# Optimization experiments

Hardware: AMD Instinct MI355X
Metric: run time of the kernel (lower is better)

Reference implementation:

```python
import jax, jax.numpy as jnp
import numpy as np

D_MODEL = 1024
N_BLOCKS = 4
D_STATE = 16
D_CONV = 4
EXPAND = 2
DT_RANK = 64  # ceil(1024/16)
D_INNER = EXPAND * D_MODEL
BATCH = 2
SEQLEN = 1024


def setup_inputs() -> dict:
    key = jax.random.key(0)
    ks = jax.random.split(key, 8)
    s = 0.02
    f = lambda k, sh: (jax.random.normal(k, sh, dtype=jnp.float32) * s)
    return {
        "x": jax.random.normal(ks[0], (BATCH, SEQLEN, D_MODEL), dtype=jnp.float32),
        "norm_w": jnp.ones((N_BLOCKS, D_MODEL), jnp.float32),
        "norm_b": jnp.zeros((N_BLOCKS, D_MODEL), jnp.float32),
        "in_proj_w": f(ks[1], (N_BLOCKS, D_MODEL, 2 * D_INNER)),
        "conv_w": f(ks[2], (N_BLOCKS, D_INNER, D_CONV)),
        "conv_b": jnp.zeros((N_BLOCKS, D_INNER), jnp.float32),
        "xproj_w": f(ks[3], (N_BLOCKS, D_INNER, DT_RANK + 2 * D_STATE)),
        "dtproj_w": f(ks[4], (N_BLOCKS, DT_RANK, D_INNER)),
        "dtproj_b": jnp.full((N_BLOCKS, D_INNER), -4.6, jnp.float32),  # softplus ~ 0.01
        "A_log": jnp.tile(jnp.log(jnp.arange(1, D_STATE + 1, dtype=jnp.float32))[None, None, :], (N_BLOCKS, D_INNER, 1)),
        "skip_D": jnp.ones((N_BLOCKS, D_INNER), jnp.float32),
        "out_proj_w": f(ks[5], (N_BLOCKS, D_INNER, D_MODEL)),
        "fn_w": jnp.ones((D_MODEL,), jnp.float32),
        "fn_b": jnp.zeros((D_MODEL,), jnp.float32),
    }


def _layer_norm(x, w, b):
    m = jnp.mean(x, -1, keepdims=True)
    v = jnp.mean((x - m) ** 2, -1, keepdims=True)
    return (x - m) * jax.lax.rsqrt(v + 1e-5) * w + b


def _selective_scan(u, dt, A, Bm, Cm, Dp):
    # u, dt: (B,L,E)  A: (E,N)  Bm, Cm: (B,L,N)  Dp: (E,)
    dA = jnp.exp(dt[..., None] * A)                 # (B,L,E,N) ZOH discretization of A
    dBu = (dt * u)[..., None] * Bm[:, :, None, :]   # (B,L,E,N) Euler discretization of B*u

    def step(h, inp):
        dA_t, dBu_t, C_t = inp
        h = dA_t * h + dBu_t                        # (B,E,N)
        y = jnp.einsum('ben,bn->be', h, C_t)
        return h, y

    h0 = jnp.zeros((u.shape[0], u.shape[2], A.shape[1]), u.dtype)
    xs = (jnp.moveaxis(dA, 1, 0), jnp.moveaxis(dBu, 1, 0), jnp.moveaxis(Cm, 1, 0))
    _, ys = jax.lax.scan(step, h0, xs)
    y = jnp.moveaxis(ys, 0, 1)                      # (B,L,E)
    return y + u * Dp


def _mamba(x, in_w, cw, cb, xw, dtw, dtb, A_log, Dp, ow):
    L = x.shape[1]
    xz = x @ in_w                                   # (B,L,2E)
    u, z = jnp.split(xz, 2, axis=-1)
    K = cw.shape[1]
    up = jnp.pad(u, ((0, 0), (K - 1, 0), (0, 0)))   # causal depthwise conv
    conv = cb + sum(up[:, k:k + L, :] * cw[:, k] for k in range(K))
    u = jax.nn.silu(conv)
    dbl = u @ xw                                    # (B,L,R+2N)
    dt = jax.nn.softplus(dbl[..., :DT_RANK] @ dtw + dtb)
    Bm = dbl[..., DT_RANK:DT_RANK + D_STATE]
    Cm = dbl[..., DT_RANK + D_STATE:]
    A = -jnp.exp(A_log)
    y = _selective_scan(u, dt, A, Bm, Cm, Dp)
    y = y * jax.nn.silu(z)                          # gating branch
    return y @ ow


def _forward(x, norm_w, norm_b, in_proj_w, conv_w, conv_b, xproj_w, dtproj_w, dtproj_b, A_log, skip_D, out_proj_w, fn_w, fn_b):
    for i in range(N_BLOCKS):
        h = _layer_norm(x, norm_w[i], norm_b[i])
        h = _mamba(h, in_proj_w[i], conv_w[i], conv_b[i], xproj_w[i], dtproj_w[i], dtproj_b[i], A_log[i], skip_D[i], out_proj_w[i])
        x = x + h                                   # pre-norm residual
    return _layer_norm(x, fn_w, fn_b)


def reference(x, norm_w, norm_b, in_proj_w, conv_w, conv_b, xproj_w, dtproj_w, dtproj_b, A_log, skip_D, out_proj_w, fn_w, fn_b):
    return _forward(x, norm_w, norm_b, in_proj_w, conv_w, conv_b, xproj_w, dtproj_w, dtproj_b, A_log, skip_D, out_proj_w, fn_w, fn_b)
```

## Files before the change

kernel.cpp:

```cpp
#include <hip/hip_runtime.h>
#include <hip/hip_bf16.h>
#include <math.h>

#define BATCH 2
#define SEQLEN 1024
#define DMODEL 1024
#define DINNER 2048
#define DSTATE 16
#define DTRANK 64
#define XDIM 96
#define KCONV 4
#define NBLOCKS 4
#define MROWS (BATCH*SEQLEN)

#define NCHUNK 64
#define CLEN (SEQLEN/NCHUNK)
#define SUN 4

typedef short bf16x8 __attribute__((ext_vector_type(8)));
typedef unsigned short u16x8 __attribute__((ext_vector_type(8)));
typedef float f32x4 __attribute__((ext_vector_type(4)));

__device__ __forceinline__ unsigned short f2bf(float x) {
    union { float f; unsigned u; } c; c.f = x;
    unsigned r = c.u + 0x7FFFu + ((c.u >> 16) & 1u);
    return (unsigned short)(r >> 16);
}
__device__ __forceinline__ float bf2f(unsigned short h) {
    union { unsigned u; float f; } c; c.u = (unsigned)h << 16;
    return c.f;
}

__device__ __forceinline__ void gload16(const void* src, void* dst) {
    __builtin_amdgcn_global_load_lds(
        (const __attribute__((address_space(1))) void*)src,
        (__attribute__((address_space(3))) void*)dst, 16, 0, 0);
}

__global__ __launch_bounds__(256) void lnc_k(const float* __restrict__ x,
    const float* __restrict__ w, const float* __restrict__ b,
    float* __restrict__ resid, unsigned short* __restrict__ out)
{
    int row = blockIdx.x;
    int tid = threadIdx.x;
    size_t off = (size_t)row * DMODEL + tid * 4;
    float4 v = *(const float4*)(x + off);
    *(float4*)(resid + off) = v;
    float s  = v.x + v.y + v.z + v.w;
    float sq = v.x*v.x + v.y*v.y + v.z*v.z + v.w*v.w;
    #pragma unroll
    for (int o = 32; o > 0; o >>= 1) {
        s  += __shfl_down(s, o);
        sq += __shfl_down(sq, o);
    }
    __shared__ float ss[4], sq4[4];
    int wid = tid >> 6;
    if ((tid & 63) == 0) { ss[wid] = s; sq4[wid] = sq; }
    __syncthreads();
    if (tid == 0) {
        ss[0]  = ss[0] + ss[1] + ss[2] + ss[3];
        sq4[0] = sq4[0] + sq4[1] + sq4[2] + sq4[3];
    }
    __syncthreads();
    float mean = ss[0] * (1.0f / DMODEL);
    float var  = sq4[0] * (1.0f / DMODEL) - mean * mean;
    float rstd = rsqrtf(var + 1e-5f);
    float4 wv = *(const float4*)(w + tid * 4);
    float4 bv = *(const float4*)(b + tid * 4);
    ushort4 h;
    h.x = f2bf((v.x - mean) * rstd * wv.x + bv.x);
    h.y = f2bf((v.y - mean) * rstd * wv.y + bv.y);
    h.z = f2bf((v.z - mean) * rstd * wv.z + bv.z);
    h.w = f2bf((v.w - mean) * rstd * wv.w + bv.w);
    *(ushort4*)(out + off) = h;
}

template<int FINAL>
__global__ __launch_bounds__(256) void predln_k(
    const float* __restrict__ pout, float* __restrict__ resid,
    const float* __restrict__ w, const float* __restrict__ b,
    unsigned short* __restrict__ hb16, float* __restrict__ fout)
{
    int row = blockIdx.x;
    int tid = threadIdx.x;
    const size_t MN = (size_t)MROWS * DMODEL;
    size_t off = (size_t)row * DMODEL + tid * 4;
    float4 p0 = *(const float4*)(pout + off);
    float4 p1 = *(const float4*)(pout + off + MN);
    float4 p2 = *(const float4*)(pout + off + 2 * MN);
    float4 p3 = *(const float4*)(pout + off + 3 * MN);
    float4 r  = *(const float4*)(resid + off);
    float4 v;
    v.x = r.x + (p0.x + p1.x) + (p2.x + p3.x);
    v.y = r.y + (p0.y + p1.y) + (p2.y + p3.y);
    v.z = r.z + (p0.z + p1.z) + (p2.z + p3.z);
    v.w = r.w + (p0.w + p1.w) + (p2.w + p3.w);
    if (!FINAL) *(float4*)(resid + off) = v;

    float s  = v.x + v.y + v.z + v.w;
    float sq = v.x*v.x + v.y*v.y + v.z*v.z + v.w*v.w;
    #pragma unroll
    for (int o = 32; o > 0; o >>= 1) {
        s  += __shfl_down(s, o);
        sq += __shfl_down(sq, o);
    }
    __shared__ float ss[4], sq4[4];
    int wid = tid >> 6;
    if ((tid & 63) == 0) { ss[wid] = s; sq4[wid] = sq; }
    __syncthreads();
    if (tid == 0) {
        ss[0]  = ss[0] + ss[1] + ss[2] + ss[3];
        sq4[0] = sq4[0] + sq4[1] + sq4[2] + sq4[3];
    }
    __syncthreads();
    float mean = ss[0] * (1.0f / DMODEL);
    float var  = sq4[0] * (1.0f / DMODEL) - mean * mean;
    float rstd = rsqrtf(var + 1e-5f);
    float4 wv = *(const float4*)(w + tid * 4);
    float4 bv = *(const float4*)(b + tid * 4);
    float o0 = (v.x - mean) * rstd * wv.x + bv.x;
    float o1 = (v.y - mean) * rstd * wv.y + bv.y;
    float o2 = (v.z - mean) * rstd * wv.z + bv.z;
    float o3 = (v.w - mean) * rstd * wv.w + bv.w;
    if (FINAL) {
        *(float4*)(fout + off) = make_float4(o0, o1, o2, o3);
    } else {
        ushort4 h;
        h.x = f2bf(o0); h.y = f2bf(o1); h.z = f2bf(o2); h.w = f2bf(o3);
        *(ushort4*)(hb16 + off) = h;
    }
}

__global__ __launch_bounds__(256) void wtr2_k(
    const float* __restrict__ W, unsigned short* __restrict__ WT,
    int N, int K, long long wstride, long long wtstride)
{
    const float* Wl = W + (size_t)blockIdx.z * wstride;
    unsigned short* WTl = WT + (size_t)blockIdx.z * wtstride;
    __shared__ float T[64][65];
    int n0 = blockIdx.x * 64, k0 = blockIdx.y * 64;
    int tid = threadIdx.x;
    int kk = tid >> 4, nn = (tid & 15) * 4;
    #pragma unroll
    for (int p = 0; p < 4; ++p) {
        float4 v = make_float4(0.f, 0.f, 0.f, 0.f);
        if (n0 + nn + 4 <= N)
            v = *(const float4*)(Wl + (size_t)(k0 + p * 16 + kk) * N + n0 + nn);
        T[p * 16 + kk][nn + 0] = v.x;
        T[p * 16 + kk][nn + 1] = v.y;
        T[p * 16 + kk][nn + 2] = v.z;
        T[p * 16 + kk][nn + 3] = v.w;
    }
    __syncthreads();
    int n2 = tid >> 4, k2 = (tid & 15) * 4;
    #pragma unroll
    for (int p = 0; p < 4; ++p) {
        int nrow = n0 + p * 16 + n2;
        ushort4 h = {0, 0, 0, 0};
        if (nrow < N) {
            h.x = f2bf(T[k2 + 0][p * 16 + n2]);
            h.y = f2bf(T[k2 + 1][p * 16 + n2]);
            h.z = f2bf(T[k2 + 2][p * 16 + n2]);
            h.w = f2bf(T[k2 + 3][p * 16 + n2]);
        }
        *(ushort4*)(WTl + (size_t)nrow * K + k0 + k2) = h;
    }
}

template<int EPI, int BN>
__global__ __launch_bounds__(256) void mgemm6_k(
    const unsigned short* __restrict__ A,
    const unsigned short* __restrict__ BT,
    float* __restrict__ out0, float* __restrict__ out1,
    const float* __restrict__ bias,
    int N, int Kf, int Kloc)
{
    constexpr int WN = BN / 2;
    constexpr int NJ = WN / 16;
    __shared__ unsigned short As[3][128 * 32];
    __shared__ unsigned short Bs[3][BN * 32];
    int tid = threadIdx.x;
    int lane = tid & 63, w = tid >> 6;
    int wr = w >> 1, wc = w & 1;
    int m0 = blockIdx.y * 128, n0 = blockIdx.x * BN;
    int lr = lane & 15, G = lane >> 4;

    int ra0 = w * 32 + (lane >> 2);
    int ra1 = ra0 + 16;
    int ga0 = (lane & 3) ^ ((ra0 >> 1) & 3);
    int ga1 = (lane & 3) ^ ((ra1 >> 1) & 3);
    int rb0 = w * (BN / 4) + (lane >> 2);
    int gb0 = (lane & 3) ^ ((rb0 >> 1) & 3);
    int rb1 = rb0 + 16;
    int gb1 = (lane & 3) ^ ((rb1 >> 1) & 3);

    int kz = blockIdx.z * Kloc;
    const unsigned short* pa0 = A  + (size_t)(m0 + ra0) * Kf + kz + ga0 * 8;
    const unsigned short* pa1 = A  + (size_t)(m0 + ra1) * Kf + kz + ga1 * 8;
    const unsigned short* pb0 = BT + (size_t)(n0 + rb0) * Kf + kz + gb0 * 8;
    const unsigned short* pb1 = BT + (size_t)(n0 + rb1) * Kf + kz + gb1 * 8;
    int dA0 = (w * 32) * 32, dA1 = dA0 + 16 * 32;
    int dB0 = (w * (BN / 4)) * 32, dB1 = dB0 + 16 * 32;

#define ISSUE(tt, bufi) do {                                   \
        gload16(pa0 + (tt) * 32, &As[bufi][dA0]);              \
        gload16(pa1 + (tt) * 32, &As[bufi][dA1]);              \
        gload16(pb0 + (tt) * 32, &Bs[bufi][dB0]);              \
        if (BN == 128) gload16(pb1 + (tt) * 32, &Bs[bufi][dB1]); \
    } while (0)

    f32x4 acc[4][NJ] = {};
    int T = Kloc / 32;

    ISSUE(0, 0);
    if (T > 1) ISSUE(1, 1);

    int cur = 0;
    for (int t = 0; t < T; ++t) {
        if (t + 1 < T) {
            if constexpr (BN == 128)
                asm volatile("s_waitcnt vmcnt(4)" ::: "memory");
            else
                asm volatile("s_waitcnt vmcnt(3)" ::: "memory");
        } else {
            asm volatile("s_waitcnt vmcnt(0)" ::: "memory");
        }
        __builtin_amdgcn_s_barrier();
        if (t + 2 < T) {
            int nb = cur + 2; if (nb >= 3) nb -= 3;
            ISSUE(t + 2, nb);
        }
        bf16x8 af[4], bfr[NJ];
        #pragma unroll
        for (int i = 0; i < 4; ++i) {
            int r = wr * 64 + i * 16 + lr;
            af[i] = *(const bf16x8*)&As[cur][r * 32 + ((G ^ ((r >> 1) & 3)) << 3)];
        }
        #pragma unroll
        for (int j = 0; j < NJ; ++j) {
            int r = wc * WN + j * 16 + lr;
            bfr[j] = *(const bf16x8*)&Bs[cur][r * 32 + ((G ^ ((r >> 1) & 3)) << 3)];
        }
        #pragma unroll
        for (int i = 0; i < 4; ++i)
            #pragma unroll
            for (int j = 0; j < NJ; ++j)
                acc[i][j] = __builtin_amdgcn_mfma_f32_16x16x32_bf16(
                    af[i], bfr[j], acc[i][j], 0, 0, 0);
        __builtin_amdgcn_s_barrier();
        cur = (cur + 1 == 3) ? 0 : cur + 1;
    }
#undef ISSUE

    int rbase = m0 + wr * 64 + (lane >> 4) * 4;
    int cbase = n0 + wc * WN + lr;
    #pragma unroll
    for (int i = 0; i < 4; ++i)
        #pragma unroll
        for (int j = 0; j < NJ; ++j)
            #pragma unroll
            for (int r = 0; r < 4; ++r) {
                int row = rbase + i * 16 + r;
                int col = cbase + j * 16;
                float c = acc[i][j][r];
                if (EPI == 0) {
                    if (col < DINNER)
                        ((unsigned short*)out0)[(size_t)row * DINNER + col] = f2bf(c);
                    else
                        ((unsigned short*)out1)[(size_t)row * DINNER + (col - DINNER)] = f2bf(c);
                } else if (EPI == 2) {
                    out0[(size_t)blockIdx.z * MROWS * N + (size_t)row * N + col] = c;
                } else if (EPI == 3) {
                    if (col < XDIM)
                        out0[(size_t)blockIdx.z * MROWS * XDIM +
                             (size_t)row * XDIM + col] = c;
                } else {
                    float cc = c + bias[col];
                    cc = fmaxf(cc, 0.f) + log1pf(__expf(-fabsf(cc)));
                    ((unsigned short*)out0)[(size_t)row * N + col] = f2bf(cc);
                }
            }
}

#define XSPLIT 16
__global__ __launch_bounds__(256) void xprojR_k(
    const float* __restrict__ part, float* __restrict__ dbl,
    unsigned short* __restrict__ db64)
{
    int idx = blockIdx.x * 256 + threadIdx.x;
    float s = 0.f;
    #pragma unroll
    for (int k = 0; k < XSPLIT; ++k)
        s += part[(size_t)k * MROWS * XDIM + idx];
    dbl[idx] = s;
    int col = idx % XDIM;
    if (col < DTRANK)
        db64[(size_t)(idx / XDIM) * DTRANK + col] = f2bf(s);
}

__global__ __launch_bounds__(256) void conv_k(const unsigned short* __restrict__ u,
    const float* __restrict__ cw, const float* __restrict__ cb,
    unsigned short* __restrict__ out)
{
    int idx = blockIdx.x * 256 + threadIdx.x;
    int c8 = idx & (DINNER / 8 - 1);
    int t  = (idx >> 8) & (SEQLEN - 1);
    int b  = idx >> 18;
    int e0 = c8 * 8;
    size_t base = (size_t)b * SEQLEN * DINNER + (size_t)t * DINNER + e0;
    u16x8 rows[KCONV];
    #pragma unroll
    for (int k = 0; k < KCONV; ++k) {
        int tt = t + k - (KCONV - 1);
        u16x8 zv = {0,0,0,0,0,0,0,0};
        rows[k] = (tt >= 0) ?
            *(const u16x8*)(u + base + (size_t)(k - (KCONV - 1)) * DINNER) : zv;
    }
    u16x8 o;
    #pragma unroll
    for (int j = 0; j < 8; ++j) {
        float4 wv = *(const float4*)(cw + (size_t)(e0 + j) * KCONV);
        float acc = cb[e0 + j];
        acc = fmaf(bf2f(rows[0][j]), wv.x, acc);
        acc = fmaf(bf2f(rows[1][j]), wv.y, acc);
        acc = fmaf(bf2f(rows[2][j]), wv.z, acc);
        acc = fmaf(bf2f(rows[3][j]), wv.w, acc);
        o[j] = f2bf(acc / (1.f + __expf(-acc)));
    }
    *(u16x8*)(out + base) = o;
}

template<int CTRL>
__device__ __forceinline__ float qadd(float x) {
    int y = __builtin_amdgcn_update_dpp(0, __float_as_int(x), CTRL, 0xF, 0xF, true);
    return x + __int_as_float(y);
}

__global__ __launch_bounds__(1024, 8) void scan_k(
    const unsigned short* __restrict__ dt, const unsigned short* __restrict__ uc,
    const float* __restrict__ dbl, const unsigned short* __restrict__ z,
    const float* __restrict__ A_log, const float* __restrict__ Dp,
    unsigned short* __restrict__ yout)
{
    __shared__ float sAlo[NCHUNK][8][2][4], sAhi[NCHUNK][8][2][4];
    __shared__ float sBlo[NCHUNK][8][2][4], sBhi[NCHUNK][8][2][4];
    int tid = threadIdx.x;
    int sub = tid & 1;
    int ei  = (tid >> 1) & 7;
    int ch  = tid >> 4;
    int bid = blockIdx.x;
    int blk = (bid & 7) * 64 + (bid >> 3);
    int eg  = blk & 255;
    int b   = blk >> 8;
    int e   = eg * 8 + ei;

    const float L2E = 1.4426950408889634f;
    float AstL2[8];
    {
        const float* ap = A_log + (size_t)e * DSTATE + sub * 8;
        #pragma unroll
        for (int q = 0; q < 2; ++q) {
            float4 v = *(const float4*)(ap + q * 4);
            AstL2[q * 4 + 0] = -__expf(v.x) * L2E;
            AstL2[q * 4 + 1] = -__expf(v.y) * L2E;
            AstL2[q * 4 + 2] = -__expf(v.z) * L2E;
            AstL2[q * 4 + 3] = -__expf(v.w) * L2E;
        }
    }
    size_t base_e = (size_t)b * SEQLEN * DINNER + e;
    size_t base_x = (size_t)b * SEQLEN * XDIM + DTRANK + sub * 8;
    int t0c = ch * CLEN;

    float h[8] = {0.f, 0.f, 0.f, 0.f, 0.f, 0.f, 0.f, 0.f};
    float ssum = 0.f;
    for (int t0 = t0c; t0 < t0c + CLEN; t0 += SUN) {
        float sdt[SUN], su[SUN];
        #pragma unroll
        for (int u = 0; u < SUN; ++u) {
            size_t te = base_e + (size_t)(t0 + u) * DINNER;
            sdt[u] = bf2f(dt[te]);
            su[u]  = bf2f(uc[te]);
        }
        #pragma unroll
        for (int u = 0; u < SUN; ++u) {
            const float* dx = dbl + base_x + (size_t)(t0 + u) * XDIM;
            float4 bn0 = *(const float4*)(dx);
            float4 bn1 = *(const float4*)(dx + 4);
            float dtu = sdt[u] * su[u];
            ssum += sdt[u];
            h[0] = fmaf(__builtin_amdgcn_exp2f(sdt[u] * AstL2[0]), h[0], dtu * bn0.x);
            h[1] = fmaf(__builtin_amdgcn_exp2f(sdt[u] * AstL2[1]), h[1], dtu * bn0.y);
            h[2] = fmaf(__builtin_amdgcn_exp2f(sdt[u] * AstL2[2]), h[2], dtu * bn0.z);
            h[3] = fmaf(__builtin_amdgcn_exp2f(sdt[u] * AstL2[3]), h[3], dtu * bn0.w);
            h[4] = fmaf(__builtin_amdgcn_exp2f(sdt[u] * AstL2[4]), h[4], dtu * bn1.x);
            h[5] = fmaf(__builtin_amdgcn_exp2f(sdt[u] * AstL2[5]), h[5], dtu * bn1.y);
            h[6] = fmaf(__builtin_amdgcn_exp2f(sdt[u] * AstL2[6]), h[6], dtu * bn1.z);
            h[7] = fmaf(__builtin_amdgcn_exp2f(sdt[u] * AstL2[7]), h[7], dtu * bn1.w);
        }
    }
    float a_[8];
    #pragma unroll
    for (int i = 0; i < 8; ++i) a_[i] = __builtin_amdgcn_exp2f(AstL2[i] * ssum);
    *(f32x4*)&sAlo[ch][ei][sub][0] = *(f32x4*)&a_[0];
    *(f32x4*)&sAhi[ch][ei][sub][0] = *(f32x4*)&a_[4];
    *(f32x4*)&sBlo[ch][ei][sub][0] = *(f32x4*)&h[0];
    *(f32x4*)&sBhi[ch][ei][sub][0] = *(f32x4*)&h[4];
    __syncthreads();

    #pragma unroll
    for (int s = 1; s < NCHUNK; s <<= 1) {
        float pa[8], pb[8];
        bool act = (ch >= s);
        if (act) {
            *(f32x4*)&pa[0] = *(const f32x4*)&sAlo[ch - s][ei][sub][0];
            *(f32x4*)&pa[4] = *(const f32x4*)&sAhi[ch - s][ei][sub][0];
            *(f32x4*)&pb[0] = *(const f32x4*)&sBlo[ch - s][ei][sub][0];
            *(f32x4*)&pb[4] = *(const f32x4*)&sBhi[ch - s][ei][sub][0];
        }
        __syncthreads();
        if (act) {
            #pragma unroll
            for (int i = 0; i < 8; ++i) {
                h[i]  = fmaf(a_[i], pb[i], h[i]);
                a_[i] *= pa[i];
            }
            *(f32x4*)&sAlo[ch][ei][sub][0] = *(f32x4*)&a_[0];
            *(f32x4*)&sAhi[ch][ei][sub][0] = *(f32x4*)&a_[4];
            *(f32x4*)&sBlo[ch][ei][sub][0] = *(f32x4*)&h[0];
            *(f32x4*)&sBhi[ch][ei][sub][0] = *(f32x4*)&h[4];
        }
        __syncthreads();
    }

    if (ch > 0) {
        *(f32x4*)&h[0] = *(const f32x4*)&sBlo[ch - 1][ei][sub][0];
        *(f32x4*)&h[4] = *(const f32x4*)&sBhi[ch - 1][ei][sub][0];
    } else {
        #pragma unroll
        for (int i = 0; i < 8; ++i) h[i] = 0.f;
    }

    float Dk = Dp[e];
    for (int t0 = t0c; t0 < t0c + CLEN; t0 += SUN) {
        float sdt[SUN], su[SUN], zz[SUN];
        #pragma unroll
        for (int u = 0; u < SUN; ++u) {
            size_t te = base_e + (size_t)(t0 + u) * DINNER;
            sdt[u] = bf2f(dt[te]);
            su[u]  = bf2f(uc[te]);
            zz[u]  = bf2f(z[te]);
        }
        #pragma unroll
        for (int u = 0; u < SUN; ++u) {
            const float* dx = dbl + base_x + (size_t)(t0 + u) * XDIM;
            float4 bn0 = *(const float4*)(dx);
            float4 bn1 = *(const float4*)(dx + 4);
            float4 cn0 = *(const float4*)(dx + 16);
            float4 cn1 = *(const float4*)(dx + 20);
            float dtu = sdt[u] * su[u];
            h[0] = fmaf(__builtin_amdgcn_exp2f(sdt[u] * AstL2[0]), h[0], dtu * bn0.x);
            h[1] = fmaf(__builtin_amdgcn_exp2f(sdt[u] * AstL2[1]), h[1], dtu * bn0.y);
            h[2] = fmaf(__builtin_amdgcn_exp2f(sdt[u] * AstL2[2]), h[2], dtu * bn0.z);
            h[3] = fmaf(__builtin_amdgcn_exp2f(sdt[u] * AstL2[3]), h[3], dtu * bn0.w);
            h[4] = fmaf(__builtin_amdgcn_exp2f(sdt[u] * AstL2[4]), h[4], dtu * bn1.x);
            h[5] = fmaf(__builtin_amdgcn_exp2f(sdt[u] * AstL2[5]), h[5], dtu * bn1.y);
            h[6] = fmaf(__builtin_amdgcn_exp2f(sdt[u] * AstL2[6]), h[6], dtu * bn1.z);
            h[7] = fmaf(__builtin_amdgcn_exp2f(sdt[u] * AstL2[7]), h[7], dtu * bn1.w);
            float p = h[0] * cn0.x + h[1] * cn0.y + h[2] * cn0.z + h[3] * cn0.w
                    + h[4] * cn1.x + h[5] * cn1.y + h[6] * cn1.z + h[7] * cn1.w;
            p = qadd<0xB1>(p);
            if (sub == 0) {
                float zvv = zz[u];
                float yv = p + su[u] * Dk;
                yout[base_e + (size_t)(t0 + u) * DINNER] =
                    f2bf(yv * (zvv / (1.f + __expf(-zvv))));
            }
        }
    }
}

extern "C" void kernel_launch(void* const* d_in, const int* in_sizes, int n_in,
                              void* d_out, int out_size, void* d_ws, size_t ws_size,
                              hipStream_t stream)
{
    const float* x         = (const float*)d_in[0];
    const float* norm_w    = (const float*)d_in[1];
    const float* norm_b    = (const float*)d_in[2];
    const float* in_proj_w = (const float*)d_in[3];
    const float* conv_w    = (const float*)d_in[4];
    const float* conv_b    = (const float*)d_in[5];
    const float* xproj_w   = (const float*)d_in[6];
    const float* dtproj_w  = (const float*)d_in[7];
    const float* dtproj_b  = (const float*)d_in[8];
    const float* A_log     = (const float*)d_in[9];
    const float* skip_D    = (const float*)d_in[10];
    const float* out_proj_w= (const float*)d_in[11];
    const float* fn_w      = (const float*)d_in[12];
    const float* fn_b      = (const float*)d_in[13];

    float* resid = (float*)d_out;
    float* ws    = (float*)d_ws;
    const size_t M1 = 1024 * 1024;
    unsigned short* wtib = (unsigned short*)(ws);
    unsigned short* wtob = (unsigned short*)(ws + 8  * M1);
    unsigned short* wtxp = (unsigned short*)(ws + 12 * M1);
    unsigned short* wtdt = (unsigned short*)(ws + 12 * M1 + M1 / 2);
    unsigned short* hb16 = (unsigned short*)(ws + 13 * M1);
    unsigned short* ub16 = (unsigned short*)(ws + 14 * M1);
    unsigned short* zb16 = (unsigned short*)(ws + 16 * M1);
    unsigned short* ucb16= (unsigned short*)(ws + 18 * M1);
    unsigned short* dtb16= (unsigned short*)(ws + 20 * M1);
    float*          dblb = ws + 22 * M1;
    unsigned short* db64 = (unsigned short*)(ws + 22 * M1 + M1 / 4);
    unsigned short* yb16 = (unsigned short*)(ws + 23 * M1);
    float*          xpart= ws + 25 * M1;
    float*          pout = ws + 28 * M1;

    wtr2_k<<<dim3(2 * DINNER / 64, DMODEL / 64, NBLOCKS), 256, 0, stream>>>(
        in_proj_w, wtib, 2 * DINNER, DMODEL,
        (long long)DMODEL * 2 * DINNER, (long long)2 * DINNER * DMODEL);
    wtr2_k<<<dim3(DMODEL / 64, DINNER / 64, NBLOCKS), 256, 0, stream>>>(
        out_proj_w, wtob, DMODEL, DINNER,
        (long long)DINNER * DMODEL, (long long)DMODEL * DINNER);
    wtr2_k<<<dim3(2, DINNER / 64, NBLOCKS), 256, 0, stream>>>(
        xproj_w, wtxp, XDIM, DINNER,
        (long long)DINNER * XDIM, (long long)128 * DINNER);
    wtr2_k<<<dim3(DINNER / 64, 1, NBLOCKS), 256, 0, stream>>>(
        dtproj_w, wtdt, DINNER, DTRANK,
        (long long)DTRANK * DINNER, (long long)DINNER * DTRANK);

    lnc_k<<<MROWS, 256, 0, stream>>>(x, norm_w, norm_b, resid, hb16);

    for (int i = 0; i < NBLOCKS; ++i) {
        mgemm6_k<0, 64><<<dim3(2 * DINNER / 64, MROWS / 128, 1), 256, 0, stream>>>(
            hb16, wtib + (size_t)i * 2 * DINNER * DMODEL,
            (float*)ub16, (float*)zb16, nullptr, 2 * DINNER, DMODEL, DMODEL);
        conv_k<<<(MROWS * DINNER / 8) / 256, 256, 0, stream>>>(
            ub16, conv_w + (size_t)i * DINNER * KCONV,
            conv_b + (size_t)i * DINNER, ucb16);
        mgemm6_k<3, 128><<<dim3(1, MROWS / 128, XSPLIT), 256, 0, stream>>>(
            ucb16, wtxp + (size_t)i * 128 * DINNER,
            xpart, nullptr, nullptr, XDIM, DINNER, DINNER / XSPLIT);
        xprojR_k<<<(MROWS * XDIM) / 256, 256, 0, stream>>>(xpart, dblb, db64);
        mgemm6_k<4, 64><<<dim3(DINNER / 64, MROWS / 128, 1), 256, 0, stream>>>(
            db64, wtdt + (size_t)i * DINNER * DTRANK,
            (float*)dtb16, nullptr, dtproj_b + (size_t)i * DINNER,
            DINNER, DTRANK, DTRANK);
        scan_k<<<BATCH * DINNER / 8, 1024, 0, stream>>>(
            dtb16, ucb16, dblb, zb16,
            A_log + (size_t)i * DINNER * DSTATE, skip_D + (size_t)i * DINNER, yb16);
        mgemm6_k<2, 64><<<dim3(DMODEL / 64, MROWS / 128, 4), 256, 0, stream>>>(
            yb16, wtob + (size_t)i * DMODEL * DINNER,
            pout, nullptr, nullptr, DMODEL, DINNER, DINNER / 4);
        if (i < NBLOCKS - 1)
            predln_k<0><<<MROWS, 256, 0, stream>>>(pout, resid,
                norm_w + (i + 1) * DMODEL, norm_b + (i + 1) * DMODEL,
                hb16, nullptr);
        else
            predln_k<1><<<MROWS, 256, 0, stream>>>(pout, resid,
                fn_w, fn_b, nullptr, resid);
    }
}
```

Before: 605.3 us.

## Store dt, z and conv output channel-major so scan reads contiguous time vectors

The GEMM epilogues for z and dt, and the conv kernel, now transpose their tiles through shared memory and write an extra (batch, channel, time) layout. The scan kernel then loads 8 consecutive timesteps per channel with one 16-byte vector load, replacing strided scalar loads. This is meant to cut the uncoalesced global traffic in the scan, at the cost of an extra transposed copy of the conv output, more LDS work, and a barrier in the epilogues. It relies on the GEMM's As buffer being large enough for a 64x136 transpose tile.

After: 772.5 us. +27.6%, slower.

```diff
diff --git a/kernel.cpp b/kernel.cpp
--- a/kernel.cpp
+++ b/kernel.cpp
@@ -15,7 +15,6 @@
 
 #define NCHUNK 64
 #define CLEN (SEQLEN/NCHUNK)
-#define SUN 4
 
 typedef short bf16x8 __attribute__((ext_vector_type(8)));
 typedef unsigned short u16x8 __attribute__((ext_vector_type(8)));
@@ -254,6 +253,44 @@
 
     int rbase = m0 + wr * 64 + (lane >> 4) * 4;
     int cbase = n0 + wc * WN + lr;
+
+    if ((EPI == 0 && n0 >= DINNER) || EPI == 6) {
+        unsigned short* Tp = (unsigned short*)As;
+        int col_l = wc * WN + (lane & 15);
+        int row_l = wr * 64 + (lane >> 4) * 4;
+        #pragma unroll
+        for (int i = 0; i < 4; ++i)
+            #pragma unroll
+            for (int j = 0; j < NJ; ++j) {
+                ushort4 h4;
+                #pragma unroll
+                for (int r = 0; r < 4; ++r) {
+                    float c = acc[i][j][r];
+                    if (EPI == 6) {
+                        c += bias[n0 + col_l + j * 16];
+                        c = fmaxf(c, 0.f) + log1pf(__expf(-fabsf(c)));
+                    }
+                    ((unsigned short*)&h4)[r] = f2bf(c);
+                }
+                *(ushort4*)&Tp[(col_l + j * 16) * 136 + row_l + i * 16] = h4;
+            }
+        __syncthreads();
+        unsigned short* dst = (EPI == 6) ? (unsigned short*)out0
+                                         : (unsigned short*)out1;
+        int e_base = (EPI == 6) ? n0 : (n0 - DINNER);
+        int er = tid >> 2, c4 = tid & 3;
+        int bb = m0 >> 10;
+        int tb = m0 & 1023;
+        #pragma unroll
+        for (int p = 0; p < 4; ++p) {
+            int tc0 = c4 * 32 + p * 8;
+            u16x8 v = *(const u16x8*)&Tp[er * 136 + tc0];
+            *(u16x8*)(dst + ((size_t)bb * DINNER + e_base + er) * SEQLEN
+                          + tb + tc0) = v;
+        }
+        return;
+    }
+
     #pragma unroll
     for (int i = 0; i < 4; ++i)
         #pragma unroll
@@ -264,20 +301,13 @@
                 int col = cbase + j * 16;
                 float c = acc[i][j][r];
                 if (EPI == 0) {
-                    if (col < DINNER)
-                        ((unsigned short*)out0)[(size_t)row * DINNER + col] = f2bf(c);
-                    else
-                        ((unsigned short*)out1)[(size_t)row * DINNER + (col - DINNER)] = f2bf(c);
+                    ((unsigned short*)out0)[(size_t)row * DINNER + col] = f2bf(c);
                 } else if (EPI == 2) {
                     out0[(size_t)blockIdx.z * MROWS * N + (size_t)row * N + col] = c;
                 } else if (EPI == 3) {
                     if (col < XDIM)
                         out0[(size_t)blockIdx.z * MROWS * XDIM +
                              (size_t)row * XDIM + col] = c;
-                } else {
-                    float cc = c + bias[col];
-                    cc = fmaxf(cc, 0.f) + log1pf(__expf(-fabsf(cc)));
-                    ((unsigned short*)out0)[(size_t)row * N + col] = f2bf(cc);
                 }
             }
 }
@@ -298,22 +328,28 @@
         db64[(size_t)(idx / XDIM) * DTRANK + col] = f2bf(s);
 }
 
-__global__ __launch_bounds__(256) void conv_k(const unsigned short* __restrict__ u,
+#define CE 32
+#define CT 64
+__global__ __launch_bounds__(256) void conv2_k(const unsigned short* __restrict__ u,
     const float* __restrict__ cw, const float* __restrict__ cb,
-    unsigned short* __restrict__ out)
-{
-    int idx = blockIdx.x * 256 + threadIdx.x;
-    int c8 = idx & (DINNER / 8 - 1);
-    int t  = (idx >> 8) & (SEQLEN - 1);
-    int b  = idx >> 18;
-    int e0 = c8 * 8;
+    unsigned short* __restrict__ uc, unsigned short* __restrict__ uct)
+{
+    __shared__ unsigned short Tl[CE * CT];
+    int tid = threadIdx.x;
+    int tt = blockIdx.x;
+    int et = blockIdx.y;
+    int b  = blockIdx.z;
+    int e8 = tid & 3;
+    int tr = tid >> 2;
+    int e0 = et * CE + e8 * 8;
+    int t  = tt * CT + tr;
     size_t base = (size_t)b * SEQLEN * DINNER + (size_t)t * DINNER + e0;
     u16x8 rows[KCONV];
     #pragma unroll
     for (int k = 0; k < KCONV; ++k) {
-        int tt = t + k - (KCONV - 1);
+        int ts = t + k - (KCONV - 1);
         u16x8 zv = {0,0,0,0,0,0,0,0};
-        rows[k] = (tt >= 0) ?
+        rows[k] = (ts >= 0) ?
             *(const u16x8*)(u + base + (size_t)(k - (KCONV - 1)) * DINNER) : zv;
     }
     u16x8 o;
@@ -327,7 +363,21 @@
         acc = fmaf(bf2f(rows[3][j]), wv.w, acc);
         o[j] = f2bf(acc / (1.f + __expf(-acc)));
     }
-    *(u16x8*)(out + base) = o;
+    *(u16x8*)(uc + base) = o;
+    #pragma unroll
+    for (int j = 0; j < 8; ++j) {
+        int e_l = e8 * 8 + j;
+        int byte = e_l * (CT * 2) + tr * 2;
+        byte ^= ((e_l >> 3) & 3) << 4;
+        *(unsigned short*)((char*)Tl + byte) = o[j];
+    }
+    __syncthreads();
+    int er = tid & 31, tc = tid >> 5;
+    int byte = er * (CT * 2) + tc * 16;
+    byte ^= ((er >> 3) & 3) << 4;
+    u16x8 v = *(const u16x8*)((char*)Tl + byte);
+    *(u16x8*)(uct + ((size_t)b * DINNER + et * CE + er) * SEQLEN
+                  + tt * CT + tc * 8) = v;
 }
 
 template<int CTRL>
@@ -337,8 +387,8 @@
 }
 
 __global__ __launch_bounds__(1024, 8) void scan_k(
-    const unsigned short* __restrict__ dt, const unsigned short* __restrict__ uc,
-    const float* __restrict__ dbl, const unsigned short* __restrict__ z,
+    const unsigned short* __restrict__ dtt, const unsigned short* __restrict__ uct,
+    const float* __restrict__ dbl, const unsigned short* __restrict__ zt,
     const float* __restrict__ A_log, const float* __restrict__ Dp,
     unsigned short* __restrict__ yout)
 {
@@ -367,35 +417,33 @@
             AstL2[q * 4 + 3] = -__expf(v.w) * L2E;
         }
     }
+    size_t base_r = ((size_t)b * DINNER + e) * SEQLEN;
     size_t base_e = (size_t)b * SEQLEN * DINNER + e;
     size_t base_x = (size_t)b * SEQLEN * XDIM + DTRANK + sub * 8;
     int t0c = ch * CLEN;
 
     float h[8] = {0.f, 0.f, 0.f, 0.f, 0.f, 0.f, 0.f, 0.f};
     float ssum = 0.f;
-    for (int t0 = t0c; t0 < t0c + CLEN; t0 += SUN) {
-        float sdt[SUN], su[SUN];
-        #pragma unroll
-        for (int u = 0; u < SUN; ++u) {
-            size_t te = base_e + (size_t)(t0 + u) * DINNER;
-            sdt[u] = bf2f(dt[te]);
-            su[u]  = bf2f(uc[te]);
-        }
-        #pragma unroll
-        for (int u = 0; u < SUN; ++u) {
+    for (int t0 = t0c; t0 < t0c + CLEN; t0 += 8) {
+        u16x8 vdt = *(const u16x8*)(dtt + base_r + t0);
+        u16x8 vu  = *(const u16x8*)(uct + base_r + t0);
+        #pragma unroll
+        for (int u = 0; u < 8; ++u) {
+            float sdt = bf2f(vdt[u]);
+            float su  = bf2f(vu[u]);
             const float* dx = dbl + base_x + (size_t)(t0 + u) * XDIM;
             float4 bn0 = *(const float4*)(dx);
             float4 bn1 = *(const float4*)(dx + 4);
-            float dtu = sdt[u] * su[u];
-            ssum += sdt[u];
-            h[0] = fmaf(__builtin_amdgcn_exp2f(sdt[u] * AstL2[0]), h[0], dtu * bn0.x);
-            h[1] = fmaf(__builtin_amdgcn_exp2f(sdt[u] * AstL2[1]), h[1], dtu * bn0.y);
-            h[2] = fmaf(__builtin_amdgcn_exp2f(sdt[u] * AstL2[2]), h[2], dtu * bn0.z);
-            h[3] = fmaf(__builtin_amdgcn_exp2f(sdt[u] * AstL2[3]), h[3], dtu * bn0.w);
-            h[4] = fmaf(__builtin_amdgcn_exp2f(sdt[u] * AstL2[4]), h[4], dtu * bn1.x);
-            h[5] = fmaf(__builtin_amdgcn_exp2f(sdt[u] * AstL2[5]), h[5], dtu * bn1.y);
-            h[6] = fmaf(__builtin_amdgcn_exp2f(sdt[u] * AstL2[6]), h[6], dtu * bn1.z);
-            h[7] = fmaf(__builtin_amdgcn_exp2f(sdt[u] * AstL2[7]), h[7], dtu * bn1.w);
+            float dtu = sdt * su;
+            ssum += sdt;
+            h[0] = fmaf(__builtin_amdgcn_exp2f(sdt * AstL2[0]), h[0], dtu * bn0.x);
+            h[1] = fmaf(__builtin_amdgcn_exp2f(sdt * AstL2[1]), h[1], dtu * bn0.y);
+            h[2] = fmaf(__builtin_amdgcn_exp2f(sdt * AstL2[2]), h[2], dtu * bn0.z);
+            h[3] = fmaf(__builtin_amdgcn_exp2f(sdt * AstL2[3]), h[3], dtu * bn0.w);
+            h[4] = fmaf(__builtin_amdgcn_exp2f(sdt * AstL2[4]), h[4], dtu * bn1.x);
+            h[5] = fmaf(__builtin_amdgcn_exp2f(sdt * AstL2[5]), h[5], dtu * bn1.y);
+            h[6] = fmaf(__builtin_amdgcn_exp2f(sdt * AstL2[6]), h[6], dtu * bn1.z);
+            h[7] = fmaf(__builtin_amdgcn_exp2f(sdt * AstL2[7]), h[7], dtu * bn1.w);
         }
     }
     float a_[8];
@@ -441,37 +489,34 @@
     }
 
     float Dk = Dp[e];
-    for (int t0 = t0c; t0 < t0c + CLEN; t0 += SUN) {
-        float sdt[SUN], su[SUN], zz[SUN];
-        #pragma unroll
-        for (int u = 0; u < SUN; ++u) {
-            size_t te = base_e + (size_t)(t0 + u) * DINNER;
-            sdt[u] = bf2f(dt[te]);
-            su[u]  = bf2f(uc[te]);
-            zz[u]  = bf2f(z[te]);
-        }
-        #pragma unroll
-        for (int u = 0; u < SUN; ++u) {
+    for (int t0 = t0c; t0 < t0c + CLEN; t0 += 8) {
+        u16x8 vdt = *(const u16x8*)(dtt + base_r + t0);
+        u16x8 vu  = *(const u16x8*)(uct + base_r + t0);
+        u16x8 vz  = *(const u16x8*)(zt  + base_r + t0);
+        #pragma unroll
+        for (int u = 0; u < 8; ++u) {
+            float sdt = bf2f(vdt[u]);
+            float su  = bf2f(vu[u]);
             const float* dx = dbl + base_x + (size_t)(t0 + u) * XDIM;
             float4 bn0 = *(const float4*)(dx);
             float4 bn1 = *(const float4*)(dx + 4);
             float4 cn0 = *(const float4*)(dx + 16);
             float4 cn1 = *(const float4*)(dx + 20);
-            float dtu = sdt[u] * su[u];
-            h[0] = fmaf(__builtin_amdgcn_exp2f(sdt[u] * AstL2[0]), h[0], dtu * bn0.x);
-            h[1] = fmaf(__builtin_amdgcn_exp2f(sdt[u] * AstL2[1]), h[1], dtu * bn0.y);
-            h[2] = fmaf(__builtin_amdgcn_exp2f(sdt[u] * AstL2[2]), h[2], dtu * bn0.z);
-            h[3] = fmaf(__builtin_amdgcn_exp2f(sdt[u] * AstL2[3]), h[3], dtu * bn0.w);
-            h[4] = fmaf(__builtin_amdgcn_exp2f(sdt[u] * AstL2[4]), h[4], dtu * bn1.x);
-            h[5] = fmaf(__builtin_amdgcn_exp2f(sdt[u] * AstL2[5]), h[5], dtu * bn1.y);
-            h[6] = fmaf(__builtin_amdgcn_exp2f(sdt[u] * AstL2[6]), h[6], dtu * bn1.z);
-            h[7] = fmaf(__builtin_amdgcn_exp2f(sdt[u] * AstL2[7]), h[7], dtu * bn1.w);
+            float dtu = sdt * su;
+            h[0] = fmaf(__builtin_amdgcn_exp2f(sdt * AstL2[0]), h[0], dtu * bn0.x);
+            h[1] = fmaf(__builtin_amdgcn_exp2f(sdt * AstL2[1]), h[1], dtu * bn0.y);
+            h[2] = fmaf(__builtin_amdgcn_exp2f(sdt * AstL2[2]), h[2], dtu * bn0.z);
+            h[3] = fmaf(__builtin_amdgcn_exp2f(sdt * AstL2[3]), h[3], dtu * bn0.w);
+            h[4] = fmaf(__builtin_amdgcn_exp2f(sdt * AstL2[4]), h[4], dtu * bn1.x);
+            h[5] = fmaf(__builtin_amdgcn_exp2f(sdt * AstL2[5]), h[5], dtu * bn1.y);
+            h[6] = fmaf(__builtin_amdgcn_exp2f(sdt * AstL2[6]), h[6], dtu * bn1.z);
+            h[7] = fmaf(__builtin_amdgcn_exp2f(sdt * AstL2[7]), h[7], dtu * bn1.w);
             float p = h[0] * cn0.x + h[1] * cn0.y + h[2] * cn0.z + h[3] * cn0.w
                     + h[4] * cn1.x + h[5] * cn1.y + h[6] * cn1.z + h[7] * cn1.w;
             p = qadd<0xB1>(p);
             if (sub == 0) {
-                float zvv = zz[u];
-                float yv = p + su[u] * Dk;
+                float zvv = bf2f(vz[u]);
+                float yv = p + su * Dk;
                 yout[base_e + (size_t)(t0 + u) * DINNER] =
                     f2bf(yv * (zvv / (1.f + __expf(-zvv))));
             }
@@ -507,14 +552,15 @@
     unsigned short* wtdt = (unsigned short*)(ws + 12 * M1 + M1 / 2);
     unsigned short* hb16 = (unsigned short*)(ws + 13 * M1);
     unsigned short* ub16 = (unsigned short*)(ws + 14 * M1);
-    unsigned short* zb16 = (unsigned short*)(ws + 16 * M1);
+    unsigned short* ztb  = (unsigned short*)(ws + 16 * M1);
     unsigned short* ucb16= (unsigned short*)(ws + 18 * M1);
-    unsigned short* dtb16= (unsigned short*)(ws + 20 * M1);
+    unsigned short* dttb = (unsigned short*)(ws + 20 * M1);
     float*          dblb = ws + 22 * M1;
     unsigned short* db64 = (unsigned short*)(ws + 22 * M1 + M1 / 4);
     unsigned short* yb16 = (unsigned short*)(ws + 23 * M1);
     float*          xpart= ws + 25 * M1;
     float*          pout = ws + 28 * M1;
+    unsigned short* uctb = (unsigned short*)(ws + 36 * M1);
 
     wtr2_k<<<dim3(2 * DINNER / 64, DMODEL / 64, NBLOCKS), 256, 0, stream>>>(
         in_proj_w, wtib, 2 * DINNER, DMODEL,
@@ -534,20 +580,20 @@
     for (int i = 0; i < NBLOCKS; ++i) {
         mgemm6_k<0, 64><<<dim3(2 * DINNER / 64, MROWS / 128, 1), 256, 0, stream>>>(
             hb16, wtib + (size_t)i * 2 * DINNER * DMODEL,
-            (float*)ub16, (float*)zb16, nullptr, 2 * DINNER, DMODEL, DMODEL);
-        conv_k<<<(MROWS * DINNER / 8) / 256, 256, 0, stream>>>(
+            (float*)ub16, (float*)ztb, nullptr, 2 * DINNER, DMODEL, DMODEL);
+        conv2_k<<<dim3(SEQLEN / CT, DINNER / CE, BATCH), 256, 0, stream>>>(
             ub16, conv_w + (size_t)i * DINNER * KCONV,
-            conv_b + (size_t)i * DINNER, ucb16);
+            conv_b + (size_t)i * DINNER, ucb16, uctb);
         mgemm6_k<3, 128><<<dim3(1, MROWS / 128, XSPLIT), 256, 0, stream>>>(
             ucb16, wtxp + (size_t)i * 128 * DINNER,
             xpart, nullptr, nullptr, XDIM, DINNER, DINNER / XSPLIT);
         xprojR_k<<<(MROWS * XDIM) / 256, 256, 0, stream>>>(xpart, dblb, db64);
-        mgemm6_k<4, 64><<<dim3(DINNER / 64, MROWS / 128, 1), 256, 0, stream>>>(
+        mgemm6_k<6, 64><<<dim3(DINNER / 64, MROWS / 128, 1), 256, 0, stream>>>(
             db64, wtdt + (size_t)i * DINNER * DTRANK,
-            (float*)dtb16, nullptr, dtproj_b + (size_t)i * DINNER,
+            (float*)dttb, nullptr, dtproj_b + (size_t)i * DINNER,
             DINNER, DTRANK, DTRANK);
         scan_k<<<BATCH * DINNER / 8, 1024, 0, stream>>>(
-            dtb16, ucb16, dblb, zb16,
+            dttb, uctb, dblb, ztb,
             A_log + (size_t)i * DINNER * DSTATE, skip_D + (size_t)i * DINNER, yb16);
         mgemm6_k<2, 64><<<dim3(DMODEL / 64, MROWS / 128, 4), 256, 0, stream>>>(
             yb16, wtob + (size_t)i * DMODEL * DINNER,
```
